# Performance work log

Measured on AMD Instinct MI355X. Metric: run time of the kernel, lower is better.

The kernel has to match this reference:

```python
import jax, jax.numpy as jnp
import numpy as np

B, N, CS, CZ, H, CH, G, P = 2, 384, 384, 128, 8, 16, 2, 8
CZ4 = CZ // 4
INF = 1e5
UMAX = 3.0     # self.u_max
LMAX = 2.0     # self.log_scale_max
SQRT_CH = CH ** 0.5


def quat_to_rot(q):
    q = q / jnp.linalg.norm(q, axis=-1, keepdims=True)
    w, x, y, z = q[..., 0], q[..., 1], q[..., 2], q[..., 3]
    R = jnp.stack([
        1 - 2 * (y * y + z * z), 2 * (x * y - w * z), 2 * (x * z + w * y),
        2 * (x * y + w * z), 1 - 2 * (x * x + z * z), 2 * (y * z - w * x),
        2 * (x * z - w * y), 2 * (y * z + w * x), 1 - 2 * (x * x + y * y)], axis=-1)
    return R.reshape(q.shape[:-1] + (3, 3))


def robust_nll(delta, sigma):
    # inline robust 3x3 Cholesky solve: dist_sq = d^T S^-1 d, log_det = ln|S|
    eps = 1e-8
    s00 = sigma[..., 0, 0]; s01 = sigma[..., 0, 1]; s02 = sigma[..., 0, 2]
    s11 = sigma[..., 1, 1]; s12 = sigma[..., 1, 2]; s22 = sigma[..., 2, 2]
    d0 = delta[..., 0]; d1 = delta[..., 1]; d2 = delta[..., 2]
    l00_sq = jnp.maximum(s00, eps); inv_l00 = jax.lax.rsqrt(l00_sq)
    l10 = s01 * inv_l00; l20 = s02 * inv_l00
    l11_sq = jnp.maximum(s11 - l10 * l10, eps); inv_l11 = jax.lax.rsqrt(l11_sq)
    l21 = (s12 - l20 * l10) * inv_l11
    l22_sq = jnp.maximum(s22 - l20 * l20 - l21 * l21, eps); inv_l22 = jax.lax.rsqrt(l22_sq)
    log_det = jnp.log(l00_sq) + jnp.log(l11_sq) + jnp.log(l22_sq)
    y0 = d0 * inv_l00
    y1 = (d1 - l10 * y0) * inv_l11
    y2 = (d2 - l20 * y0 - l21 * y1) * inv_l22
    return y0 * y0 + y1 * y1 + y2 * y2, log_det


def iga_forward(s, z, mask, rot, trans, local_mean, scaling_log,
                Wq, Wk, Wv, Wb, bb, Wdz, bdz, Wqg, bqg, Wkg, bkg,
                Wvp, bvp, geo_scale, geo_bias, Wout, bout):
    # scalar q/k/v: [B,H,N,CH]
    q = (s @ Wq).reshape(B, N, H, CH).transpose(0, 2, 1, 3)
    k = (s @ Wk).reshape(B, N, H, CH).transpose(0, 2, 1, 3)
    v = (s @ Wv).reshape(B, N, H, CH).transpose(0, 2, 1, 3)
    logits = jnp.einsum('bhid,bhjd->bhij', q, k) / SQRT_CH
    # pair bias: [B,H,N,N]
    logits = logits + (z @ Wb + bb).transpose(0, 3, 1, 2)

    def parse(feat):  # -> u [B,N,H,G,3], s_log_delta [B,N,H,G,3]
        raw = feat.reshape(B, N, H, G, 6)
        return jnp.tanh(raw[..., :3]) * UMAX, jnp.tanh(raw[..., 3:]) * LMAX

    def to_global(u, sld):
        anchor = local_mean[:, :, None, None, :]
        base = scaling_log[:, :, None, None, :]
        sig_loc = jnp.maximum(jnp.exp(base + sld), 1e-6)
        pos = anchor + u * sig_loc
        mu = jnp.einsum('bnij,bnhgj->bnhgi', rot, pos) + trans[:, :, None, None, :]
        var = jnp.exp(2.0 * (base + sld))
        Sig = jnp.einsum('bnij,bnhgj,bnkj->bnhgik', rot, var, rot)  # R diag(var) R^T
        return mu.transpose(0, 2, 1, 3, 4), Sig.transpose(0, 2, 1, 3, 4, 5)

    qu, qs = parse(s @ Wqg + bqg)
    ku, ks = parse(s @ Wkg + bkg)
    q_mu, q_sig = to_global(qu, qs)   # [B,H,N,G,3], [B,H,N,G,3,3]
    k_mu, k_sig = to_global(ku, ks)
    delta = q_mu[:, :, :, None] - k_mu[:, :, None, :]      # [B,H,N,N,G,3]
    ssum = q_sig[:, :, :, None] + k_sig[:, :, None, :]     # [B,H,N,N,G,3,3]
    dist_sq, log_det = robust_nll(delta, ssum)
    geo = (-0.5 * dist_sq - 0.5 * log_det).sum(-1)          # [B,H,N,N]

    mask2d = mask[:, None, :, None] * mask[:, None, None, :]  # [B,1,N,N]
    a = jax.nn.softplus(geo_scale)[None, :, None, None]
    G_geo = a * (geo * mask2d) + geo_bias[None, :, None, None]
    logits = logits + G_geo + (1.0 - mask2d) * (-INF)
    w = jax.nn.softmax(logits, axis=-1)                      # [B,H,N,N]

    # scalar output
    o = jnp.einsum('bhij,bhjd->bihd', w, v).reshape(B, N, H * CH)
    # point output (IPA-style): to global, attend, back to local frame
    vpts = (s @ Wvp + bvp).reshape(B, N, H, P, 3)
    vpg = jnp.einsum('bnij,bnhpj->bnhpi', rot, vpts) + trans[:, :, None, None, :]
    vpg = vpg.transpose(0, 2, 1, 3, 4)                       # [B,H,N,P,3]
    opt = jnp.einsum('bhij,bhjpc->bhipc', w, vpg)            # [B,H,N,P,3]
    opt_local = jnp.einsum('bnji,bhnpj->bnhpi', rot, opt - trans[:, None, :, None, :])
    onorm = jnp.sqrt((opt_local ** 2).sum(-1) + 1e-8)        # [B,N,H,P]
    # pair output
    pz = z @ Wdz + bdz                                       # [B,N,N,CZ4]
    opair = jnp.einsum('bhij,bijc->bihc', w, pz)             # [B,N,H,CZ4]

    cat = jnp.concatenate([o, opt_local.reshape(B, N, H * P * 3),
                           onorm.reshape(B, N, H * P),
                           opair.reshape(B, N, H * CZ4)], axis=-1)  # [B,N,640]
    return cat @ Wout + bout


def setup_inputs() -> dict:
    ks = jax.random.split(jax.random.key(0), 24)
    rnd = lambda i, shape, sc=1.0: jax.random.normal(ks[i], shape, dtype=jnp.float32) * sc
    w = 0.02
    return dict(
        s=rnd(0, (B, N, CS)), z=rnd(1, (B, N, N, CZ)),
        mask=jnp.ones((B, N), jnp.float32),
        rot=quat_to_rot(rnd(2, (B, N, 4))),
        trans=rnd(3, (B, N, 3), 1.0),
        local_mean=rnd(4, (B, N, 3), 0.5),
        scaling_log=rnd(5, (B, N, 3), 0.1),
        Wq=rnd(6, (CS, H * CH), w), Wk=rnd(7, (CS, H * CH), w), Wv=rnd(8, (CS, H * CH), w),
        Wb=rnd(9, (CZ, H), w), bb=rnd(10, (H,), w),
        Wdz=rnd(11, (CZ, CZ4), w), bdz=rnd(12, (CZ4,), w),
        Wqg=rnd(13, (CS, H * G * 6), w), bqg=rnd(14, (H * G * 6,), w),
        Wkg=rnd(15, (CS, H * G * 6), w), bkg=rnd(16, (H * G * 6,), w),
        Wvp=rnd(17, (CS, H * P * 3), w), bvp=rnd(18, (H * P * 3,), w),
        geo_scale=jnp.ones((H,), jnp.float32), geo_bias=jnp.zeros((H,), jnp.float32),
        Wout=rnd(19, (H * (CH + P * 4 + CZ4), CS), w), bout=jnp.zeros((CS,), jnp.float32))


def reference(s, z, mask, rot, trans, local_mean, scaling_log, Wq, Wk, Wv, Wb, bb,
              Wdz, bdz, Wqg, bqg, Wkg, bkg, Wvp, bvp, geo_scale, geo_bias, Wout, bout):
    return iga_forward(s, z, mask, rot, trans, local_mean, scaling_log, Wq, Wk, Wv,
                       Wb, bb, Wdz, bdz, Wqg, bqg, Wkg, bkg, Wvp, bvp,
                       geo_scale, geo_bias, Wout, bout)
```

## Files before the change

kernel.cpp:

```cpp
#include <hip/hip_runtime.h>
#include <hip/hip_fp16.h>

#define NB   2
#define NN   384
#define NCS  384
#define NCZ  128
#define NH   8
#define NCH  16
#define NG   2
#define NP   8
#define NCZ4 32
#define BN   (NB*NN)
#define LINW 768
#define PZROW ((size_t)BN*NN)
#define NZB  (BN*6)
#define NRB  288

typedef _Float16 f16x8 __attribute__((ext_vector_type(8)));
typedef float    f32x4 __attribute__((ext_vector_type(4)));

typedef __attribute__((address_space(3))) char        as3_char;
typedef __attribute__((address_space(1))) const char  as1_char;
static __device__ __forceinline__ void gload_lds16(const void* g, void* l) {
    __builtin_amdgcn_global_load_lds((const as1_char*)g, (as3_char*)l, 16, 0, 0);
}

__global__ void k_wprep(const float* __restrict__ Wb, const float* __restrict__ Wdz,
                        _Float16* __restrict__ wf) {
    int t = threadIdx.x;
    for (int e = t; e < 12*64*8; e += 256) {
        int r = e & 7, lane = (e >> 3) & 63, nk = e >> 9;
        int n = nk >> 2, kk = nk & 3;
        int c = kk*32 + (lane >> 4)*8 + r;
        int col = n*16 + (lane & 15);
        float w;
        if      (col < 8)  w = Wb[c*NH + col];
        else if (col < 40) w = Wdz[c*NCZ4 + (col-8)];
        else               w = 0.f;
        wf[e] = (_Float16)w;
    }
}

__global__ void k_zrow(const float* __restrict__ z, const _Float16* __restrict__ wf,
       const float* __restrict__ bb, const float* __restrict__ bdz,
       const float* __restrict__ s,
       const float* __restrict__ Wq, const float* __restrict__ Wk,
       const float* __restrict__ Wv,
       const float* __restrict__ Wqg, const float* __restrict__ bqg,
       const float* __restrict__ Wkg, const float* __restrict__ bkg,
       const float* __restrict__ Wvp, const float* __restrict__ bvp,
       float* __restrict__ zbg, __half* __restrict__ pzg2,
       float* __restrict__ lin, float* __restrict__ kT, float* __restrict__ vT) {
    __shared__ __align__(16) char smem[39168];
    int t = threadIdx.x;

    if (blockIdx.x >= NRB) {
        int lane = t & 63, w = t >> 6;
        int ccol = lane & 15;
        int cjl  = w*16 + (lane >> 4)*4;
        int zb = blockIdx.x - NRB;
        int bi = zb / 6, ch = zb % 6;
        const char* zbase = (const char*)(z + ((size_t)bi*NN + ch*64)*NCZ);

        #pragma unroll
        for (int i = 0; i < 8; ++i) {
            int o = (w*8 + i)*1024 + lane*16;
            int r = o >> 9;
            int u = (o >> 4) & 31;
            const char* src = zbase + (r << 9) + ((u ^ (r & 7)) << 4);
            char* dst = smem + (w*8 + i)*1024;
            gload_lds16(src, dst);
        }

        f16x8 bfr[12];
        #pragma unroll
        for (int nk = 0; nk < 12; ++nk)
            bfr[nk] = ((const f16x8*)wf)[nk*64 + lane];

        float b0 = (ccol < 8) ? bb[ccol] : bdz[ccol - 8];
        float b1 = bdz[ccol + 8];
        float b2 = (ccol < 8) ? bdz[ccol + 24] : 0.f;

        asm volatile("s_waitcnt vmcnt(0)");
        __syncthreads();

        int row = w*16 + (lane & 15);
        int r7  = row & 7;
        const char* zrow_b = smem + row*512;
        f16x8 af0, af1, af2, af3;
        {
            int u0;
            float4 lo, hi;
            #define LD_FRAG(AF, KK)                                                   \
                u0 = ((lane >> 4) << 1) + (KK)*8;                                     \
                lo = *(const float4*)(zrow_b + (((u0    ) ^ r7) << 4));               \
                hi = *(const float4*)(zrow_b + (((u0 + 1) ^ r7) << 4));               \
                AF[0]=(_Float16)lo.x; AF[1]=(_Float16)lo.y;                           \
                AF[2]=(_Float16)lo.z; AF[3]=(_Float16)lo.w;                           \
                AF[4]=(_Float16)hi.x; AF[5]=(_Float16)hi.y;                           \
                AF[6]=(_Float16)hi.z; AF[7]=(_Float16)hi.w;
            LD_FRAG(af0, 0)
            LD_FRAG(af1, 1)
            LD_FRAG(af2, 2)
            LD_FRAG(af3, 3)
            #undef LD_FRAG
        }

        f32x4 ac0 = {0.f,0.f,0.f,0.f}, ac1 = ac0, ac2 = ac0;
        ac0 = __builtin_amdgcn_mfma_f32_16x16x32_f16(af0, bfr[0], ac0, 0,0,0);
        ac1 = __builtin_amdgcn_mfma_f32_16x16x32_f16(af0, bfr[4], ac1, 0,0,0);
        ac2 = __builtin_amdgcn_mfma_f32_16x16x32_f16(af0, bfr[8], ac2, 0,0,0);
        ac0 = __builtin_amdgcn_mfma_f32_16x16x32_f16(af1, bfr[1], ac0, 0,0,0);
        ac1 = __builtin_amdgcn_mfma_f32_16x16x32_f16(af1, bfr[5], ac1, 0,0,0);
        ac2 = __builtin_amdgcn_mfma_f32_16x16x32_f16(af1, bfr[9], ac2, 0,0,0);
        ac0 = __builtin_amdgcn_mfma_f32_16x16x32_f16(af2, bfr[2], ac0, 0,0,0);
        ac1 = __builtin_amdgcn_mfma_f32_16x16x32_f16(af2, bfr[6], ac1, 0,0,0);
        ac2 = __builtin_amdgcn_mfma_f32_16x16x32_f16(af2, bfr[10], ac2, 0,0,0);
        ac0 = __builtin_amdgcn_mfma_f32_16x16x32_f16(af3, bfr[3], ac0, 0,0,0);
        ac1 = __builtin_amdgcn_mfma_f32_16x16x32_f16(af3, bfr[7], ac1, 0,0,0);
        ac2 = __builtin_amdgcn_mfma_f32_16x16x32_f16(af3, bfr[11], ac2, 0,0,0);

        float (*zbT)[64] = (float(*)[64])(smem + 32768);
        __half (*pzt)[34] = (__half(*)[34])(smem + 32768 + 2048);
        #pragma unroll
        for (int r = 0; r < 4; ++r) {
            int j = cjl + r;
            float v0 = ac0[r] + b0;
            if (ccol < 8) zbT[ccol][j] = v0;
            else          pzt[j][ccol-8] = __float2half(v0);
            pzt[j][ccol+8] = __float2half(ac1[r] + b1);
            if (ccol < 8)
                pzt[j][ccol+24] = __float2half(ac2[r] + b2);
        }
        __syncthreads();

        {
            int e = t*2, h = e >> 6, j = e & 63;
            float2 v; v.x = zbT[h][j]; v.y = zbT[h][j+1];
            *(float2*)(zbg + ((size_t)bi*NH + h)*NN + ch*64 + j) = v;
        }
        {
            int cp = t >> 4, l = t & 15, j0 = l*4;
            union { __half2 h2[4]; float4 f4; } u;
            #pragma unroll
            for (int r = 0; r < 4; ++r) {
                int j = j0 + r;
                u.h2[r] = __halves2half2(pzt[j][2*cp], pzt[j][2*cp+1]);
            }
            __half2* dst = (__half2*)pzg2 + (size_t)cp*PZROW + (size_t)bi*NN + ch*64 + j0;
            *(float4*)dst = u.f4;
        }
    } else {
        float (*sl)[NCS] = (float(*)[NCS])smem;
        int rb = blockIdx.x;
        int r0 = (rb / 3) * 8;
        int col = (rb % 3) * 256 + t;
        for (int idx = t; idx < 8*NCS; idx += 256)
            sl[idx / NCS][idx % NCS] = s[(size_t)(r0 + idx/NCS)*NCS + (idx % NCS)];
        __syncthreads();
        const float* W; int sw; float bias = 0.f;
        if      (col < 128) { W = Wq  + col;        sw = 128; }
        else if (col < 256) { W = Wk  + (col-128);  sw = 128; }
        else if (col < 384) { W = Wv  + (col-256);  sw = 128; }
        else if (col < 480) { W = Wqg + (col-384);  sw = 96;  bias = bqg[col-384]; }
        else if (col < 576) { W = Wkg + (col-480);  sw = 96;  bias = bkg[col-480]; }
        else                { W = Wvp + (col-576);  sw = 192; bias = bvp[col-576]; }
        float a[8];
        #pragma unroll
        for (int r = 0; r < 8; ++r) a[r] = 0.f;
        #pragma unroll 1
        for (int c = 0; c < NCS; c += 4) {
            float w0 = W[(size_t)(c+0)*sw];
            float w1 = W[(size_t)(c+1)*sw];
            float w2 = W[(size_t)(c+2)*sw];
            float w3 = W[(size_t)(c+3)*sw];
            #pragma unroll
            for (int r = 0; r < 8; ++r) {
                a[r] = fmaf(sl[r][c+0], w0, a[r]);
                a[r] = fmaf(sl[r][c+1], w1, a[r]);
                a[r] = fmaf(sl[r][c+2], w2, a[r]);
                a[r] = fmaf(sl[r][c+3], w3, a[r]);
            }
        }
        #pragma unroll
        for (int r = 0; r < 8; ++r)
            lin[(size_t)(r0+r)*LINW + col] = a[r] + bias;
        if (col >= 128 && col < 384) {
            f32x4 v0, v1;
            #pragma unroll
            for (int r = 0; r < 4; ++r) { v0[r] = a[r]; v1[r] = a[4+r]; }
            float* dst = (col < 256) ? (kT + (size_t)(col-128)*BN + r0)
                                     : (vT + (size_t)(col-256)*BN + r0);
            *(f32x4*)dst = v0;
            *(f32x4*)(dst+4) = v1;
        }
    }
}

__global__ void k_geom(const float* __restrict__ lin, const float* __restrict__ rot,
                       const float* __restrict__ trans, const float* __restrict__ lm,
                       const float* __restrict__ sc,
                       float* __restrict__ qmu, float* __restrict__ qsig,
                       float* __restrict__ kmuT, float* __restrict__ ksigT,
                       float* __restrict__ vpgT) {
    int bn = blockIdx.x, t = threadIdx.x;
    __shared__ float R[9], T[3], A[3], Bs[3];
    if (t < 9) R[t] = rot[bn*9 + t];
    if (t < 3) { T[t] = trans[bn*3+t]; A[t] = lm[bn*3+t]; Bs[t] = sc[bn*3+t]; }
    __syncthreads();
    {
        int h = t >> 3, p = t & 7;
        const float* vr = lin + (size_t)bn*LINW + 576 + h*24 + p*3;
        float x = vr[0], y = vr[1], z = vr[2];
        int e = h*24 + p*3;
        vpgT[(size_t)(e+0)*BN + bn] = R[0]*x + R[1]*y + R[2]*z + T[0];
        vpgT[(size_t)(e+1)*BN + bn] = R[3]*x + R[4]*y + R[5]*z + T[1];
        vpgT[(size_t)(e+2)*BN + bn] = R[6]*x + R[7]*y + R[8]*z + T[2];
    }
    if (t < 32) {
        int side = t >> 4, item = t & 15;
        const float* raw = lin + (size_t)bn*LINW + (side ? 480 : 384) + item*6;
        float u0 = tanhf(raw[0])*3.f, u1 = tanhf(raw[1])*3.f, u2 = tanhf(raw[2])*3.f;
        float e0 = Bs[0] + tanhf(raw[3])*2.f;
        float e1 = Bs[1] + tanhf(raw[4])*2.f;
        float e2 = Bs[2] + tanhf(raw[5])*2.f;
        float sl0 = fmaxf(expf(e0), 1e-6f);
        float sl1 = fmaxf(expf(e1), 1e-6f);
        float sl2 = fmaxf(expf(e2), 1e-6f);
        float p0 = A[0] + u0*sl0, p1 = A[1] + u1*sl1, p2 = A[2] + u2*sl2;
        float mu0 = R[0]*p0 + R[1]*p1 + R[2]*p2 + T[0];
        float mu1 = R[3]*p0 + R[4]*p1 + R[5]*p2 + T[1];
        float mu2 = R[6]*p0 + R[7]*p1 + R[8]*p2 + T[2];
        float v0 = expf(2.f*e0), v1 = expf(2.f*e1), v2 = expf(2.f*e2);
        float s00 = R[0]*R[0]*v0 + R[1]*R[1]*v1 + R[2]*R[2]*v2;
        float s01 = R[0]*R[3]*v0 + R[1]*R[4]*v1 + R[2]*R[5]*v2;
        float s02 = R[0]*R[6]*v0 + R[1]*R[7]*v1 + R[2]*R[8]*v2;
        float s11 = R[3]*R[3]*v0 + R[4]*R[4]*v1 + R[5]*R[5]*v2;
        float s12 = R[3]*R[6]*v0 + R[4]*R[7]*v1 + R[5]*R[8]*v2;
        float s22 = R[6]*R[6]*v0 + R[7]*R[7]*v1 + R[8]*R[8]*v2;
        if (side) {
            kmuT[(size_t)(item*3+0)*BN + bn] = mu0;
            kmuT[(size_t)(item*3+1)*BN + bn] = mu1;
            kmuT[(size_t)(item*3+2)*BN + bn] = mu2;
            ksigT[(size_t)(item*6+0)*BN + bn] = s00;
            ksigT[(size_t)(item*6+1)*BN + bn] = s01;
            ksigT[(size_t)(item*6+2)*BN + bn] = s02;
            ksigT[(size_t)(item*6+3)*BN + bn] = s11;
            ksigT[(size_t)(item*6+4)*BN + bn] = s12;
            ksigT[(size_t)(item*6+5)*BN + bn] = s22;
        } else {
            float* mud = qmu + (size_t)bn*48 + item*3;
            mud[0]=mu0; mud[1]=mu1; mud[2]=mu2;
            float* sgd = qsig + (size_t)bn*96 + item*6;
            sgd[0]=s00; sgd[1]=s01; sgd[2]=s02; sgd[3]=s11; sgd[4]=s12; sgd[5]=s22;
        }
    }
}

__global__ void __launch_bounds__(256, 2)
k_attn2(const float* __restrict__ mask,
        const float* __restrict__ rot, const float* __restrict__ trans,
        const float* __restrict__ lin,
        const float* __restrict__ qmu, const float* __restrict__ qsig,
        const float* __restrict__ kmuT, const float* __restrict__ ksigT,
        const float* __restrict__ kT, const float* __restrict__ vT,
        const float* __restrict__ vpgT,
        const float* __restrict__ zbg, const __half* __restrict__ pzg2,
        const float* __restrict__ gsc, const float* __restrict__ gbi,
        float* __restrict__ cat) {
    __shared__ float  logits[NH][NN];
    __shared__ float  qrow[128];
    __shared__ float  qmu_s[48], qsig_s[96];
    __shared__ float  Rm[9], Tv[3];
    __shared__ float  aH[NH], bH[NH];
    __shared__ float  maskI;

    int t  = threadIdx.x;
    int b  = blockIdx.x / NN, i = blockIdx.x % NN;
    int bi = b*NN + i;
    const size_t boff = (size_t)b*NN;

    if (t < 128) qrow[t] = lin[(size_t)bi*LINW + t];
    if (t < 48)  qmu_s[t] = qmu[(size_t)bi*48 + t];
    if (t >= 64 && t < 160) qsig_s[t-64] = qsig[(size_t)bi*96 + (t-64)];
    if (t >= 160 && t < 169) Rm[t-160] = rot[bi*9 + (t-160)];
    if (t >= 169 && t < 172) Tv[t-169] = trans[bi*3 + (t-169)];
    if (t >= 176 && t < 184) {
        int h = t-176;
        float x = gsc[h];
        aH[h] = (x > 20.f) ? x : log1pf(expf(x));
        bH[h] = gbi[h];
    }
    if (t == 255) maskI = mask[bi];
    __syncthreads();

    int h = t >> 5, lnn = t & 31;
    {
        float qv[16];
        #pragma unroll
        for (int d = 0; d < 16; ++d) qv[d] = qrow[h*16 + d];
        float qm[6], qs[12];
        #pragma unroll
        for (int e = 0; e < 6; ++e)  qm[e] = qmu_s[h*6 + e];
        #pragma unroll
        for (int e = 0; e < 12; ++e) qs[e] = qsig_s[h*12 + e];
        float ascale = aH[h], hbias = bH[h], mI = maskI;
        #pragma unroll 1
        for (int jj = 0; jj < 3; ++jj) {
            int j4 = jj*128 + lnn*4;
            const float* kp = kT + (size_t)(h*16)*BN + boff + j4;
            f32x4 qk = {0.f,0.f,0.f,0.f};
            #pragma unroll
            for (int d = 0; d < 16; ++d) {
                f32x4 kv = *(const f32x4*)(kp + (size_t)d*BN);
                #pragma unroll
                for (int r = 0; r < 4; ++r) qk[r] = fmaf(qv[d], kv[r], qk[r]);
            }
            f32x4 geo = {0.f,0.f,0.f,0.f};
            #pragma unroll
            for (int g = 0; g < NG; ++g) {
                const float* kmb = kmuT + (size_t)((h*2+g)*3)*BN + boff + j4;
                f32x4 km0 = *(const f32x4*)(kmb);
                f32x4 km1 = *(const f32x4*)(kmb + BN);
                f32x4 km2 = *(const f32x4*)(kmb + 2*BN);
                const float* ksb = ksigT + (size_t)((h*2+g)*6)*BN + boff + j4;
                f32x4 ks0 = *(const f32x4*)(ksb);
                f32x4 ks1 = *(const f32x4*)(ksb + BN);
                f32x4 ks2 = *(const f32x4*)(ksb + 2*BN);
                f32x4 ks3 = *(const f32x4*)(ksb + 3*BN);
                f32x4 ks4 = *(const f32x4*)(ksb + 4*BN);
                f32x4 ks5 = *(const f32x4*)(ksb + 5*BN);
                #pragma unroll
                for (int r = 0; r < 4; ++r) {
                    float d0 = qm[g*3+0] - km0[r];
                    float d1 = qm[g*3+1] - km1[r];
                    float d2 = qm[g*3+2] - km2[r];
                    float s00 = qs[g*6+0] + ks0[r];
                    float s01 = qs[g*6+1] + ks1[r];
                    float s02 = qs[g*6+2] + ks2[r];
                    float s11 = qs[g*6+3] + ks3[r];
                    float s12 = qs[g*6+4] + ks4[r];
                    float s22 = qs[g*6+5] + ks5[r];
                    float l00 = fmaxf(s00, 1e-8f);
                    float i00 = rsqrtf(l00);
                    float l10 = s01*i00, l20 = s02*i00;
                    float l11 = fmaxf(s11 - l10*l10, 1e-8f);
                    float i11 = rsqrtf(l11);
                    float l21 = (s12 - l20*l10)*i11;
                    float l22 = fmaxf(s22 - l20*l20 - l21*l21, 1e-8f);
                    float i22 = rsqrtf(l22);
                    float ld = __logf(l00) + __logf(l11) + __logf(l22);
                    float y0 = d0*i00;
                    float y1 = (d1 - l10*y0)*i11;
                    float y2 = (d2 - l20*y0 - l21*y1)*i22;
                    geo[r] += -0.5f*(y0*y0 + y1*y1 + y2*y2 + ld);
                }
            }
            f32x4 zb4 = *(const f32x4*)(zbg + ((size_t)bi*NH + h)*NN + j4);
            f32x4 mv  = *(const f32x4*)(mask + boff + j4);
            f32x4 lg;
            #pragma unroll
            for (int r = 0; r < 4; ++r) {
                float m2 = mI * mv[r];
                lg[r] = qk[r]*0.25f + zb4[r] + ascale*(geo[r]*m2) + hbias
                        + (1.f - m2)*(-100000.f);
            }
            *(f32x4*)&logits[h][j4] = lg;
        }
    }
    __syncthreads();

    float mx = -3.4e38f;
    #pragma unroll
    for (int jj = 0; jj < 12; ++jj) mx = fmaxf(mx, logits[h][lnn + jj*32]);
    #pragma unroll
    for (int m = 16; m >= 1; m >>= 1) mx = fmaxf(mx, __shfl_xor(mx, m, 64));
    float se = 0.f;
    #pragma unroll
    for (int jj = 0; jj < 12; ++jj) {
        int j = lnn + jj*32;
        float e = __expf(logits[h][j] - mx);
        logits[h][j] = e;
        se += e;
    }
    #pragma unroll
    for (int m = 16; m >= 1; m >>= 1) se += __shfl_xor(se, m, 64);
    float inv = 1.f / se;
    float* cp = cat + (size_t)bi*640;

    {
        float o[16];
        #pragma unroll
        for (int d = 0; d < 16; ++d) o[d] = 0.f;
        const float* vbase = vT + (size_t)(h*16)*BN + boff;
        #pragma unroll 1
        for (int jj = 0; jj < 3; ++jj) {
            int j4 = jj*128 + lnn*4;
            f32x4 lg4 = *(const f32x4*)&logits[h][j4];
            f32x4 w4;
            #pragma unroll
            for (int r = 0; r < 4; ++r) w4[r] = lg4[r] * inv;
            const float* vb = vbase + j4;
            #pragma unroll
            for (int d = 0; d < 16; ++d) {
                f32x4 kv = *(const f32x4*)(vb + (size_t)d*BN);
                #pragma unroll
                for (int r = 0; r < 4; ++r) o[d] = fmaf(w4[r], kv[r], o[d]);
            }
        }
        #pragma unroll
        for (int m = 16; m >= 1; m >>= 1) {
            #pragma unroll
            for (int d = 0; d < 16; ++d) o[d] += __shfl_xor(o[d], m, 64);
        }
        if (lnn == 0) {
            #pragma unroll
            for (int d = 0; d < 16; ++d) cp[h*16 + d] = o[d];
        }
    }

    {
        float op[24];
        #pragma unroll
        for (int e = 0; e < 24; ++e) op[e] = 0.f;
        const float* gbase = vpgT + (size_t)(h*24)*BN + boff;
        #pragma unroll 1
        for (int jj = 0; jj < 3; ++jj) {
            int j4 = jj*128 + lnn*4;
            f32x4 lg4 = *(const f32x4*)&logits[h][j4];
            f32x4 w4;
            #pragma unroll
            for (int r = 0; r < 4; ++r) w4[r] = lg4[r] * inv;
            const float* gb = gbase + j4;
            #pragma unroll
            for (int e = 0; e < 24; ++e) {
                f32x4 gv = *(const f32x4*)(gb + (size_t)e*BN);
                #pragma unroll
                for (int r = 0; r < 4; ++r) op[e] = fmaf(w4[r], gv[r], op[e]);
            }
        }
        #pragma unroll
        for (int m = 16; m >= 1; m >>= 1) {
            #pragma unroll
            for (int e = 0; e < 24; ++e) op[e] += __shfl_xor(op[e], m, 64);
        }
        if (lnn == 0) {
            #pragma unroll
            for (int p = 0; p < 8; ++p) {
                float x  = op[p*3+0] - Tv[0];
                float y  = op[p*3+1] - Tv[1];
                float zz = op[p*3+2] - Tv[2];
                float l0 = Rm[0]*x + Rm[3]*y + Rm[6]*zz;
                float l1 = Rm[1]*x + Rm[4]*y + Rm[7]*zz;
                float l2 = Rm[2]*x + Rm[5]*y + Rm[8]*zz;
                cp[128 + h*24 + p*3 + 0] = l0;
                cp[128 + h*24 + p*3 + 1] = l1;
                cp[128 + h*24 + p*3 + 2] = l2;
                cp[320 + h*8 + p] = sqrtf(l0*l0 + l1*l1 + l2*l2 + 1e-8f);
            }
        }
    }

    {
        float opa[32];
        #pragma unroll
        for (int c = 0; c < 32; ++c) opa[c] = 0.f;
        const __half2* pzb = (const __half2*)pzg2 + (size_t)bi*NN;
        #pragma unroll 1
        for (int jj = 0; jj < 3; ++jj) {
            int j4 = jj*128 + lnn*4;
            f32x4 lg4 = *(const f32x4*)&logits[h][j4];
            f32x4 w4;
            #pragma unroll
            for (int r = 0; r < 4; ++r) w4[r] = lg4[r] * inv;
            #pragma unroll
            for (int c2 = 0; c2 < 16; ++c2) {
                union { float4 f4; __half2 h2[4]; } u;
                u.f4 = *(const float4*)(pzb + (size_t)c2*PZROW + j4);
                #pragma unroll
                for (int r = 0; r < 4; ++r) {
                    float2 pf = __half22float2(u.h2[r]);
                    opa[2*c2]   = fmaf(w4[r], pf.x, opa[2*c2]);
                    opa[2*c2+1] = fmaf(w4[r], pf.y, opa[2*c2+1]);
                }
            }
        }
        #pragma unroll
        for (int m = 16; m >= 1; m >>= 1) {
            #pragma unroll
            for (int c = 0; c < 32; ++c) opa[c] += __shfl_xor(opa[c], m, 64);
        }
        if (lnn == 0) {
            #pragma unroll
            for (int c = 0; c < 32; ++c) cp[384 + h*32 + c] = opa[c];
        }
    }
}

__global__ void k_out(const float* __restrict__ cat, const float* __restrict__ Wout,
                      const float* __restrict__ bout, float* __restrict__ out) {
    __shared__ float cl[4][640];
    int t  = threadIdx.x;
    int r0 = blockIdx.x * 4;
    for (int idx = t; idx < 4*640; idx += 384)
        cl[idx/640][idx%640] = cat[(size_t)(r0 + idx/640)*640 + (idx%640)];
    __syncthreads();
    int col = t;
    float a0=0.f, a1=0.f, a2=0.f, a3=0.f;
    for (int c = 0; c < 640; ++c) {
        float w = Wout[(size_t)c*NCS + col];
        a0 = fmaf(cl[0][c], w, a0);
        a1 = fmaf(cl[1][c], w, a1);
        a2 = fmaf(cl[2][c], w, a2);
        a3 = fmaf(cl[3][c], w, a3);
    }
    float bv = bout[col];
    out[(size_t)(r0+0)*NCS + col] = a0 + bv;
    out[(size_t)(r0+1)*NCS + col] = a1 + bv;
    out[(size_t)(r0+2)*NCS + col] = a2 + bv;
    out[(size_t)(r0+3)*NCS + col] = a3 + bv;
}

extern "C" void kernel_launch(void* const* d_in, const int* in_sizes, int n_in,
                              void* d_out, int out_size, void* d_ws, size_t ws_size,
                              hipStream_t stream) {
    const float* s    = (const float*)d_in[0];
    const float* z    = (const float*)d_in[1];
    const float* mask = (const float*)d_in[2];
    const float* rot  = (const float*)d_in[3];
    const float* trans= (const float*)d_in[4];
    const float* lm   = (const float*)d_in[5];
    const float* sc   = (const float*)d_in[6];
    const float* Wq   = (const float*)d_in[7];
    const float* Wk   = (const float*)d_in[8];
    const float* Wv   = (const float*)d_in[9];
    const float* Wb   = (const float*)d_in[10];
    const float* bb   = (const float*)d_in[11];
    const float* Wdz  = (const float*)d_in[12];
    const float* bdz  = (const float*)d_in[13];
    const float* Wqg  = (const float*)d_in[14];
    const float* bqg  = (const float*)d_in[15];
    const float* Wkg  = (const float*)d_in[16];
    const float* bkg  = (const float*)d_in[17];
    const float* Wvp  = (const float*)d_in[18];
    const float* bvp  = (const float*)d_in[19];
    const float* gsc  = (const float*)d_in[20];
    const float* gbi  = (const float*)d_in[21];
    const float* Wout = (const float*)d_in[22];
    const float* bout = (const float*)d_in[23];
    float* out = (float*)d_out;

    float* ws    = (float*)d_ws;
    float* lin   = ws;
    float* qmu   = lin   + 589824;
    float* qsig  = qmu   + 36864;
    float* kmuT  = qsig  + 73728;
    float* ksigT = kmuT  + 36864;
    float* vpgT  = ksigT + 73728;
    float* kT    = vpgT  + 147456;
    float* vT    = kT    + 98304;
    float* cat   = vT    + 98304;
    float* zbg   = cat   + 491520;
    __half* pzg2 = (__half*)(zbg + 2359296);
    _Float16* wf = (_Float16*)((float*)pzg2 + 4718592);

    k_wprep<<<1, 256, 0, stream>>>(Wb, Wdz, wf);
    k_zrow<<<NRB + NZB, 256, 0, stream>>>(z, wf, bb, bdz, s,
                                          Wq, Wk, Wv, Wqg, bqg, Wkg, bkg, Wvp, bvp,
                                          zbg, pzg2, lin, kT, vT);
    k_geom<<<BN, 64, 0, stream>>>(lin, rot, trans, lm, sc, qmu, qsig, kmuT, ksigT, vpgT);
    k_attn2<<<BN, 256, 0, stream>>>(mask, rot, trans, lin, qmu, qsig, kmuT, ksigT,
                                    kT, vT, vpgT, zbg, pzg2, gsc, gbi, cat);
    k_out<<<192, 384, 0, stream>>>(cat, Wout, bout, out);
}
```

Before: 146.7 us.

## Double-buffer z chunk DMA in k_zrow with four chunks per block

The z-projection part of k_zrow now launches a quarter as many blocks, and each block processes four 64-row chunks. Two LDS buffers are used so the global-to-LDS copy of the next chunk overlaps the MFMA and store work on the current one. The B-fragment and bias loads are done once per block instead of once per chunk. The cost is that the shared allocation doubles to about 78 KB for every block, including the s-projection blocks, which lowers how many blocks can sit on a CU at once.

```diff
diff --git a/kernel.cpp b/kernel.cpp
--- a/kernel.cpp
+++ b/kernel.cpp
@@ -13,7 +13,7 @@
 #define BN   (NB*NN)
 #define LINW 768
 #define PZROW ((size_t)BN*NN)
-#define NZB  (BN*6)
+#define NZP  1152
 #define NRB  288
 
 typedef _Float16 f16x8 __attribute__((ext_vector_type(8)));
@@ -41,6 +41,84 @@
     }
 }
 
+static __device__ __forceinline__ void zchunk_body(
+        const char* zbuf, char* outb, const f16x8* bfr,
+        float b0, float b1, float b2,
+        int t, int lane, int w, int ccol, int cjl, int bi, int ch,
+        float* __restrict__ zbg, __half* __restrict__ pzg2) {
+    float (*zbT)[64] = (float(*)[64])outb;
+    __half (*pzt)[34] = (__half(*)[34])(outb + 2048);
+    int row = w*16 + (lane & 15);
+    int r7  = row & 7;
+    const char* zrow_b = zbuf + row*512;
+    f16x8 af[4];
+    #pragma unroll
+    for (int kk = 0; kk < 4; ++kk) {
+        int u0 = ((lane >> 4) << 1) + kk*8;
+        float4 lo = *(const float4*)(zrow_b + (((u0    ) ^ r7) << 4));
+        float4 hi = *(const float4*)(zrow_b + (((u0 + 1) ^ r7) << 4));
+        af[kk][0]=(_Float16)lo.x; af[kk][1]=(_Float16)lo.y;
+        af[kk][2]=(_Float16)lo.z; af[kk][3]=(_Float16)lo.w;
+        af[kk][4]=(_Float16)hi.x; af[kk][5]=(_Float16)hi.y;
+        af[kk][6]=(_Float16)hi.z; af[kk][7]=(_Float16)hi.w;
+    }
+    f32x4 ac0 = {0.f,0.f,0.f,0.f}, ac1 = ac0, ac2 = ac0;
+    ac0 = __builtin_amdgcn_mfma_f32_16x16x32_f16(af[0], bfr[0], ac0, 0,0,0);
+    ac1 = __builtin_amdgcn_mfma_f32_16x16x32_f16(af[0], bfr[4], ac1, 0,0,0);
+    ac2 = __builtin_amdgcn_mfma_f32_16x16x32_f16(af[0], bfr[8], ac2, 0,0,0);
+    ac0 = __builtin_amdgcn_mfma_f32_16x16x32_f16(af[1], bfr[1], ac0, 0,0,0);
+    ac1 = __builtin_amdgcn_mfma_f32_16x16x32_f16(af[1], bfr[5], ac1, 0,0,0);
+    ac2 = __builtin_amdgcn_mfma_f32_16x16x32_f16(af[1], bfr[9], ac2, 0,0,0);
+    ac0 = __builtin_amdgcn_mfma_f32_16x16x32_f16(af[2], bfr[2], ac0, 0,0,0);
+    ac1 = __builtin_amdgcn_mfma_f32_16x16x32_f16(af[2], bfr[6], ac1, 0,0,0);
+    ac2 = __builtin_amdgcn_mfma_f32_16x16x32_f16(af[2], bfr[10], ac2, 0,0,0);
+    ac0 = __builtin_amdgcn_mfma_f32_16x16x32_f16(af[3], bfr[3], ac0, 0,0,0);
+    ac1 = __builtin_amdgcn_mfma_f32_16x16x32_f16(af[3], bfr[7], ac1, 0,0,0);
+    ac2 = __builtin_amdgcn_mfma_f32_16x16x32_f16(af[3], bfr[11], ac2, 0,0,0);
+    #pragma unroll
+    for (int r = 0; r < 4; ++r) {
+        int j = cjl + r;
+        float v0 = ac0[r] + b0;
+        if (ccol < 8) zbT[ccol][j] = v0;
+        else          pzt[j][ccol-8] = __float2half(v0);
+        pzt[j][ccol+8] = __float2half(ac1[r] + b1);
+        if (ccol < 8)
+            pzt[j][ccol+24] = __float2half(ac2[r] + b2);
+    }
+    asm volatile("s_waitcnt lgkmcnt(0)" ::: "memory");
+    __builtin_amdgcn_sched_barrier(0);
+    __builtin_amdgcn_s_barrier();
+    __builtin_amdgcn_sched_barrier(0);
+    {
+        int e = t*2, h = e >> 6, j = e & 63;
+        float2 v; v.x = zbT[h][j]; v.y = zbT[h][j+1];
+        *(float2*)(zbg + ((size_t)bi*NH + h)*NN + ch*64 + j) = v;
+    }
+    {
+        int cp = t >> 4, l = t & 15, j0 = l*4;
+        union { __half2 h2[4]; float4 f4; } u;
+        #pragma unroll
+        for (int r = 0; r < 4; ++r) {
+            int j = j0 + r;
+            u.h2[r] = __halves2half2(pzt[j][2*cp], pzt[j][2*cp+1]);
+        }
+        __half2* dst = (__half2*)pzg2 + (size_t)cp*PZROW + (size_t)bi*NN + ch*64 + j0;
+        *(float4*)dst = u.f4;
+    }
+}
+
+static __device__ __forceinline__ void dma_chunk(const float* z, int c, int lane, int w,
+                                                 char* dstbuf) {
+    const char* nb = (const char*)(z + ((size_t)(c/6)*NN + (c%6)*64)*NCZ);
+    #pragma unroll
+    for (int i = 0; i < 8; ++i) {
+        int o = (w*8 + i)*1024 + lane*16;
+        int r = o >> 9;
+        int u = (o >> 4) & 31;
+        gload_lds16(nb + (r << 9) + ((u ^ (r & 7)) << 4), dstbuf + (w*8 + i)*1024);
+    }
+}
+
 __global__ void k_zrow(const float* __restrict__ z, const _Float16* __restrict__ wf,
        const float* __restrict__ bb, const float* __restrict__ bdz,
        const float* __restrict__ s,
@@ -51,104 +129,63 @@
        const float* __restrict__ Wvp, const float* __restrict__ bvp,
        float* __restrict__ zbg, __half* __restrict__ pzg2,
        float* __restrict__ lin, float* __restrict__ kT, float* __restrict__ vT) {
-    __shared__ __align__(16) char smem[39168];
+    __shared__ __align__(16) char smem[78336];
     int t = threadIdx.x;
 
     if (blockIdx.x >= NRB) {
         int lane = t & 63, w = t >> 6;
         int ccol = lane & 15;
         int cjl  = w*16 + (lane >> 4)*4;
-        int zb = blockIdx.x - NRB;
-        int bi = zb / 6, ch = zb % 6;
-        const char* zbase = (const char*)(z + ((size_t)bi*NN + ch*64)*NCZ);
-
-        #pragma unroll
-        for (int i = 0; i < 8; ++i) {
-            int o = (w*8 + i)*1024 + lane*16;
-            int r = o >> 9;
-            int u = (o >> 4) & 31;
-            const char* src = zbase + (r << 9) + ((u ^ (r & 7)) << 4);
-            char* dst = smem + (w*8 + i)*1024;
-            gload_lds16(src, dst);
-        }
+        int zbid = blockIdx.x - NRB;
+
+        dma_chunk(z, zbid, lane, w, smem);
 
         f16x8 bfr[12];
         #pragma unroll
         for (int nk = 0; nk < 12; ++nk)
             bfr[nk] = ((const f16x8*)wf)[nk*64 + lane];
-
         float b0 = (ccol < 8) ? bb[ccol] : bdz[ccol - 8];
         float b1 = bdz[ccol + 8];
         float b2 = (ccol < 8) ? bdz[ccol + 24] : 0.f;
 
-        asm volatile("s_waitcnt vmcnt(0)");
-        __syncthreads();
-
-        int row = w*16 + (lane & 15);
-        int r7  = row & 7;
-        const char* zrow_b = smem + row*512;
-        f16x8 af0, af1, af2, af3;
+        dma_chunk(z, zbid + NZP, lane, w, smem + 32768);
+        asm volatile("s_waitcnt vmcnt(8)" ::: "memory");
+        __builtin_amdgcn_sched_barrier(0);
+        __builtin_amdgcn_s_barrier();
+        __builtin_amdgcn_sched_barrier(0);
+        zchunk_body(smem, smem + 65536, bfr, b0, b1, b2, t, lane, w, ccol, cjl,
+                    zbid / 6, zbid % 6, zbg, pzg2);
+
+        dma_chunk(z, zbid + 2*NZP, lane, w, smem);
+        asm volatile("s_waitcnt vmcnt(8)" ::: "memory");
+        __builtin_amdgcn_sched_barrier(0);
+        __builtin_amdgcn_s_barrier();
+        __builtin_amdgcn_sched_barrier(0);
         {
-            int u0;
-            float4 lo, hi;
-            #define LD_FRAG(AF, KK)                                                   \
-                u0 = ((lane >> 4) << 1) + (KK)*8;                                     \
-                lo = *(const float4*)(zrow_b + (((u0    ) ^ r7) << 4));               \
-                hi = *(const float4*)(zrow_b + (((u0 + 1) ^ r7) << 4));               \
-                AF[0]=(_Float16)lo.x; AF[1]=(_Float16)lo.y;                           \
-                AF[2]=(_Float16)lo.z; AF[3]=(_Float16)lo.w;                           \
-                AF[4]=(_Float16)hi.x; AF[5]=(_Float16)hi.y;                           \
-                AF[6]=(_Float16)hi.z; AF[7]=(_Float16)hi.w;
-            LD_FRAG(af0, 0)
-            LD_FRAG(af1, 1)
-            LD_FRAG(af2, 2)
-            LD_FRAG(af3, 3)
-            #undef LD_FRAG
-        }
-
-        f32x4 ac0 = {0.f,0.f,0.f,0.f}, ac1 = ac0, ac2 = ac0;
-        ac0 = __builtin_amdgcn_mfma_f32_16x16x32_f16(af0, bfr[0], ac0, 0,0,0);
-        ac1 = __builtin_amdgcn_mfma_f32_16x16x32_f16(af0, bfr[4], ac1, 0,0,0);
-        ac2 = __builtin_amdgcn_mfma_f32_16x16x32_f16(af0, bfr[8], ac2, 0,0,0);
-        ac0 = __builtin_amdgcn_mfma_f32_16x16x32_f16(af1, bfr[1], ac0, 0,0,0);
-        ac1 = __builtin_amdgcn_mfma_f32_16x16x32_f16(af1, bfr[5], ac1, 0,0,0);
-        ac2 = __builtin_amdgcn_mfma_f32_16x16x32_f16(af1, bfr[9], ac2, 0,0,0);
-        ac0 = __builtin_amdgcn_mfma_f32_16x16x32_f16(af2, bfr[2], ac0, 0,0,0);
-        ac1 = __builtin_amdgcn_mfma_f32_16x16x32_f16(af2, bfr[6], ac1, 0,0,0);
-        ac2 = __builtin_amdgcn_mfma_f32_16x16x32_f16(af2, bfr[10], ac2, 0,0,0);
-        ac0 = __builtin_amdgcn_mfma_f32_16x16x32_f16(af3, bfr[3], ac0, 0,0,0);
-        ac1 = __builtin_amdgcn_mfma_f32_16x16x32_f16(af3, bfr[7], ac1, 0,0,0);
-        ac2 = __builtin_amdgcn_mfma_f32_16x16x32_f16(af3, bfr[11], ac2, 0,0,0);
-
-        float (*zbT)[64] = (float(*)[64])(smem + 32768);
-        __half (*pzt)[34] = (__half(*)[34])(smem + 32768 + 2048);
-        #pragma unroll
-        for (int r = 0; r < 4; ++r) {
-            int j = cjl + r;
-            float v0 = ac0[r] + b0;
-            if (ccol < 8) zbT[ccol][j] = v0;
-            else          pzt[j][ccol-8] = __float2half(v0);
-            pzt[j][ccol+8] = __float2half(ac1[r] + b1);
-            if (ccol < 8)
-                pzt[j][ccol+24] = __float2half(ac2[r] + b2);
-        }
-        __syncthreads();
-
+            int c = zbid + NZP;
+            zchunk_body(smem + 32768, smem + 65536 + 6400, bfr, b0, b1, b2, t, lane, w,
+                        ccol, cjl, c / 6, c % 6, zbg, pzg2);
+        }
+
+        dma_chunk(z, zbid + 3*NZP, lane, w, smem + 32768);
+        asm volatile("s_waitcnt vmcnt(8)" ::: "memory");
+        __builtin_amdgcn_sched_barrier(0);
+        __builtin_amdgcn_s_barrier();
+        __builtin_amdgcn_sched_barrier(0);
         {
-            int e = t*2, h = e >> 6, j = e & 63;
-            float2 v; v.x = zbT[h][j]; v.y = zbT[h][j+1];
-            *(float2*)(zbg + ((size_t)bi*NH + h)*NN + ch*64 + j) = v;
-        }
+            int c = zbid + 2*NZP;
+            zchunk_body(smem, smem + 65536, bfr, b0, b1, b2, t, lane, w,
+                        ccol, cjl, c / 6, c % 6, zbg, pzg2);
+        }
+
+        asm volatile("s_waitcnt vmcnt(0)" ::: "memory");
+        __builtin_amdgcn_sched_barrier(0);
+        __builtin_amdgcn_s_barrier();
+        __builtin_amdgcn_sched_barrier(0);
         {
-            int cp = t >> 4, l = t & 15, j0 = l*4;
-            union { __half2 h2[4]; float4 f4; } u;
-            #pragma unroll
-            for (int r = 0; r < 4; ++r) {
-                int j = j0 + r;
-                u.h2[r] = __halves2half2(pzt[j][2*cp], pzt[j][2*cp+1]);
-            }
-            __half2* dst = (__half2*)pzg2 + (size_t)cp*PZROW + (size_t)bi*NN + ch*64 + j0;
-            *(float4*)dst = u.f4;
+            int c = zbid + 3*NZP;
+            zchunk_body(smem + 32768, smem + 65536 + 6400, bfr, b0, b1, b2, t, lane, w,
+                        ccol, cjl, c / 6, c % 6, zbg, pzg2);
         }
     } else {
         float (*sl)[NCS] = (float(*)[NCS])smem;
@@ -565,7 +602,7 @@
     _Float16* wf = (_Float16*)((float*)pzg2 + 4718592);
 
     k_wprep<<<1, 256, 0, stream>>>(Wb, Wdz, wf);
-    k_zrow<<<NRB + NZB, 256, 0, stream>>>(z, wf, bb, bdz, s,
+    k_zrow<<<NRB + NZP, 256, 0, stream>>>(z, wf, bb, bdz, s,
                                           Wq, Wk, Wv, Wqg, bqg, Wkg, bkg, Wvp, bvp,
                                           zbg, pzg2, lin, kT, vT);
     k_geom<<<BN, 64, 0, stream>>>(lin, rot, trans, lm, sc, qmu, qsig, kmuT, ksigT, vpgT);
```

After: 146.0 us, median of 2. Within noise of the previous version (-0.5%).
